# Optimization experiments

Measured on AMD Instinct MI355X. Metric: run time of the kernel, lower is better.

## Reference

```python
import jax, jax.numpy as jnp
import numpy as np

N = 100_000   # nodes
E = 1_600_000 # edges
IN, HID, OUT = 128, 64, 32


def _glorot(key, fan_in, fan_out):
    s = jnp.sqrt(6.0 / (fan_in + fan_out)).astype(jnp.float32)
    return jax.random.uniform(key, (fan_in, fan_out), jnp.float32, -s, s)


def setup_inputs() -> dict:
    key = jax.random.key(0)
    ks = jax.random.split(key, 8)
    x = jax.random.normal(ks[0], (N, IN), jnp.float32)
    edge_index = jax.random.randint(ks[1], (2, E), 0, N, jnp.int64)
    return {
        "x": x,
        "edge_index": edge_index,
        "W1": _glorot(ks[2], IN, HID),
        "b1": jnp.zeros((HID,), jnp.float32),
        "W_mu": _glorot(ks[3], HID, OUT),
        "b_mu": jnp.zeros((OUT,), jnp.float32),
        "W_ls": _glorot(ks[4], HID, OUT),
        "b_ls": jnp.zeros((OUT,), jnp.float32),
    }


def _gcn_conv(x, W, b, src, dst, n, dinv_sqrt):
    """PyG GCNConv: h = x @ W; symmetric-normalized scatter-add incl. self-loops; + b."""
    h = x @ W                                       # [N, F_out]
    coef = dinv_sqrt[src] * dinv_sqrt[dst]          # [E]
    msg = h[src] * coef[:, None]                    # [E, F_out] gather
    agg = jax.ops.segment_sum(msg, dst, num_segments=n)  # scatter-add
    agg = agg + h * (dinv_sqrt * dinv_sqrt)[:, None]      # self-loop contribution
    return agg + b


def reference(x, edge_index, W1, b1, W_mu, b_mu, W_ls, b_ls):
    src, dst = edge_index[0], edge_index[1]
    n = x.shape[0]
    # degree on graph with self-loops (edge weight 1), shared by all three convs
    deg = jax.ops.segment_sum(jnp.ones((src.shape[0],), x.dtype), dst, num_segments=n) + 1.0
    dinv_sqrt = jax.lax.rsqrt(deg)
    h = jax.nn.relu(_gcn_conv(x, W1, b1, src, dst, n, dinv_sqrt))
    mu = _gcn_conv(h, W_mu, b_mu, src, dst, n, dinv_sqrt)
    logstd = _gcn_conv(h, W_ls, b_ls, src, dst, n, dinv_sqrt)
    return mu, logstd
```

## Files before the change

kernel.cpp:

```cpp
#include <hip/hip_runtime.h>
#include <hip/hip_bf16.h>

#define FIN 128
#define HID 64
#define BSN 128
#define BSHIFT 7
#define SRCBITS 20
#define EPB 8192

typedef __attribute__((ext_vector_type(8))) short short8;
typedef __attribute__((ext_vector_type(4))) float floatx4;

__device__ __forceinline__ float bf2f(unsigned short u) {
    union { unsigned int i; float f; } c;
    c.i = ((unsigned int)u) << 16;
    return c.f;
}

__device__ __forceinline__ unsigned short f2bf(float f) {
    union { float f; unsigned int i; } c;
    c.f = f;
    unsigned int u = c.i;
    unsigned int r = (u + 0x7FFFu + ((u >> 16) & 1u)) >> 16;
    return (unsigned short)r;
}

__global__ void bin_count(const int* __restrict__ dst, int* __restrict__ bcnt,
                          int E, int B) {
    __shared__ int hist[1024];
    for (int i = threadIdx.x; i < 1024; i += 256) hist[i] = 0;
    __syncthreads();
    int base = blockIdx.x * EPB;
    int lim = min(base + EPB, E);
    for (int e = base + threadIdx.x; e < lim; e += 256)
        atomicAdd(&hist[dst[e] >> BSHIFT], 1);
    __syncthreads();
    for (int b = threadIdx.x; b < B; b += 256)
        if (hist[b]) atomicAdd(&bcnt[b], hist[b]);
}

__global__ void scan_bkt(int* __restrict__ bcnt, int* __restrict__ bbase,
                         int E, int B) {
    __shared__ int s[1024];
    int t = threadIdx.x;
    int v = (t < B) ? bcnt[t] : 0;
    s[t] = v;
    __syncthreads();
    for (int off = 1; off < 1024; off <<= 1) {
        int a = (t >= off) ? s[t - off] : 0;
        __syncthreads();
        s[t] += a;
        __syncthreads();
    }
    if (t < B) { int ex = s[t] - v; bbase[t] = ex; bcnt[t] = ex; }
    if (t == 0) bbase[B] = E;
}

__global__ void bin_fill(const int* __restrict__ src, const int* __restrict__ dst,
                         int* __restrict__ bcur, unsigned* __restrict__ rec, int E) {
    __shared__ int hist[1024];
    __shared__ int cbase[1024];
    for (int i = threadIdx.x; i < 1024; i += 256) hist[i] = 0;
    __syncthreads();
    int base = blockIdx.x * EPB;
    int lim = min(base + EPB, E);
    for (int e = base + threadIdx.x; e < lim; e += 256)
        atomicAdd(&hist[dst[e] >> BSHIFT], 1);
    __syncthreads();
    for (int b = threadIdx.x; b < 1024; b += 256) {
        int c = hist[b];
        cbase[b] = c ? atomicAdd(&bcur[b], c) : 0;
    }
    __syncthreads();
    for (int i = threadIdx.x; i < 1024; i += 256) hist[i] = 0;
    __syncthreads();
    for (int e = base + threadIdx.x; e < lim; e += 256) {
        int d = dst[e];
        int b = d >> BSHIFT;
        int slot = atomicAdd(&hist[b], 1);
        rec[cbase[b] + slot] = (unsigned)src[e] | ((unsigned)(d & (BSN - 1)) << SRCBITS);
    }
}

__global__ void csr_build(const unsigned* __restrict__ rec, const int* __restrict__ bbase,
                          int* __restrict__ row, int* __restrict__ rend,
                          int* __restrict__ csr, float* __restrict__ dinv, int N) {
    __shared__ int cnt[BSN], excl[BSN], cur[BSN];
    int b = blockIdx.x, t = threadIdx.x;
    if (t < BSN) cnt[t] = 0;
    __syncthreads();
    int start = bbase[b], end = bbase[b + 1];
    for (int i = start + t; i < end; i += 256)
        atomicAdd(&cnt[rec[i] >> SRCBITS], 1);
    __syncthreads();
    if (t < BSN) excl[t] = cnt[t];
    __syncthreads();
    for (int off = 1; off < BSN; off <<= 1) {
        int a = 0;
        if (t < BSN && t >= off) a = excl[t - off];
        __syncthreads();
        if (t < BSN) excl[t] += a;
        __syncthreads();
    }
    if (t < BSN) {
        int inc = excl[t];
        int ex = inc - cnt[t];
        excl[t] = ex;
        cur[t] = 0;
        int n = b * BSN + t;
        if (n < N) {
            row[n]  = start + ex;
            rend[n] = start + inc;
            dinv[n] = rsqrtf((float)cnt[t] + 1.0f);
        }
    }
    __syncthreads();
    for (int i = start + t; i < end; i += 256) {
        unsigned r = rec[i];
        int dl = r >> SRCBITS;
        int slot = atomicAdd(&cur[dl], 1);
        csr[start + excl[dl] + slot] = (int)(r & ((1u << SRCBITS) - 1));
    }
}

__global__ __launch_bounds__(256) void gemm1_mfma(
    const float* __restrict__ x, const float* __restrict__ W1,
    const float* __restrict__ dinv, unsigned short* __restrict__ h0, int N) {
    int wave = threadIdx.x >> 6, lane = threadIdx.x & 63;
    int m = lane & 15, q = lane >> 4;
    short8 bfr[4][4];
#pragma unroll
    for (int ct = 0; ct < 4; ++ct)
#pragma unroll
        for (int kk = 0; kk < 4; ++kk) {
            short8 tf;
#pragma unroll
            for (int jj = 0; jj < 8; ++jj)
                tf[jj] = (short)f2bf(W1[(kk * 32 + q * 8 + jj) * HID + ct * 16 + m]);
            bfr[ct][kk] = tf;
        }
    int ntiles = N >> 4;
    for (int t = blockIdx.x * 4 + wave; t < ntiles; t += gridDim.x * 4) {
        int nbase = t << 4;
        const float* xr = x + (size_t)(nbase + m) * FIN + q * 8;
        short8 afr[4];
#pragma unroll
        for (int kk = 0; kk < 4; ++kk) {
            float4 p0 = *((const float4*)(xr + kk * 32));
            float4 p1 = *((const float4*)(xr + kk * 32 + 4));
            short8 ta;
            ta[0] = (short)f2bf(p0.x); ta[1] = (short)f2bf(p0.y);
            ta[2] = (short)f2bf(p0.z); ta[3] = (short)f2bf(p0.w);
            ta[4] = (short)f2bf(p1.x); ta[5] = (short)f2bf(p1.y);
            ta[6] = (short)f2bf(p1.z); ta[7] = (short)f2bf(p1.w);
            afr[kk] = ta;
        }
        floatx4 cacc[4];
#pragma unroll
        for (int ct = 0; ct < 4; ++ct) cacc[ct] = floatx4{0.f, 0.f, 0.f, 0.f};
#pragma unroll
        for (int ct = 0; ct < 4; ++ct)
#pragma unroll
            for (int kk = 0; kk < 4; ++kk)
                cacc[ct] = __builtin_amdgcn_mfma_f32_16x16x32_bf16(afr[kk], bfr[ct][kk], cacc[ct], 0, 0, 0);
        float4 dv = *((const float4*)(dinv + nbase + q * 4));
#pragma unroll
        for (int ct = 0; ct < 4; ++ct) {
#pragma unroll
            for (int r = 0; r < 4; ++r) {
                float d = (r == 0) ? dv.x : (r == 1) ? dv.y : (r == 2) ? dv.z : dv.w;
                int n = nbase + q * 4 + r;
                h0[(size_t)n * HID + ct * 16 + m] = f2bf(cacc[ct][r] * d);
            }
        }
    }
}

__global__ void pull(const unsigned short* __restrict__ hp,
                     const int* __restrict__ row, const int* __restrict__ rend,
                     const int* __restrict__ csr, const float* __restrict__ dinv,
                     const float* __restrict__ b1,
                     unsigned short* __restrict__ outp, int N, int mode) {
    int wave = threadIdx.x >> 6, lane = threadIdx.x & 63;
    int n = blockIdx.x * 4 + wave;
    if (n >= N) return;
    int start = __builtin_amdgcn_readfirstlane(row[n]);
    int end   = __builtin_amdgcn_readfirstlane(rend[n]);
    float a0 = 0.f, a1 = 0.f, a2 = 0.f, a3 = 0.f;
    float a4 = 0.f, a5 = 0.f, a6 = 0.f, a7 = 0.f;
    int j = start;
    for (; j + 8 <= end; j += 8) {
        int s0 = csr[j],     s1 = csr[j + 1], s2 = csr[j + 2], s3 = csr[j + 3];
        int s4 = csr[j + 4], s5 = csr[j + 5], s6 = csr[j + 6], s7 = csr[j + 7];
        a0 += bf2f(hp[(size_t)s0 * HID + lane]);
        a1 += bf2f(hp[(size_t)s1 * HID + lane]);
        a2 += bf2f(hp[(size_t)s2 * HID + lane]);
        a3 += bf2f(hp[(size_t)s3 * HID + lane]);
        a4 += bf2f(hp[(size_t)s4 * HID + lane]);
        a5 += bf2f(hp[(size_t)s5 * HID + lane]);
        a6 += bf2f(hp[(size_t)s6 * HID + lane]);
        a7 += bf2f(hp[(size_t)s7 * HID + lane]);
    }
    for (; j < end; ++j) {
        int s = csr[j];
        a0 += bf2f(hp[(size_t)s * HID + lane]);
    }
    float acc = ((a0 + a1) + (a2 + a3)) + ((a4 + a5) + (a6 + a7));
    acc += bf2f(hp[(size_t)n * HID + lane]);
    float di = dinv[n];
    float v;
    if (mode == 0) {
        v = di * acc + b1[lane];
        v = v > 0.f ? v : 0.f;
        v *= di;
    } else {
        v = di * acc;
    }
    outp[(size_t)n * HID + lane] = f2bf(v);
}

__global__ __launch_bounds__(256, 4) void gemm2_mfma(
    const unsigned short* __restrict__ abar,
    const float* __restrict__ Wmu, const float* __restrict__ bmu,
    const float* __restrict__ Wls, const float* __restrict__ bls,
    float* __restrict__ out, int N) {
    int wave = threadIdx.x >> 6, lane = threadIdx.x & 63;
    int m = lane & 15, q = lane >> 4;
    short8 bfr[4][2];
#pragma unroll
    for (int ct = 0; ct < 4; ++ct)
#pragma unroll
        for (int kk = 0; kk < 2; ++kk) {
            short8 tf;
#pragma unroll
            for (int jj = 0; jj < 8; ++jj) {
                int k = kk * 32 + q * 8 + jj;
                int col = ct * 16 + m;
                float w = (col < 32) ? Wmu[k * 32 + col] : Wls[k * 32 + (col - 32)];
                tf[jj] = (short)f2bf(w);
            }
            bfr[ct][kk] = tf;
        }
    float bias[4];
#pragma unroll
    for (int ct = 0; ct < 4; ++ct) {
        int col = ct * 16 + m;
        bias[ct] = (col < 32) ? bmu[col] : bls[col - 32];
    }
    int ntiles = N >> 4;
    int gw = blockIdx.x * 4 + wave;
    int nw = gridDim.x * 4;
    for (int t = gw; t < ntiles; t += nw) {
        int nbase = t << 4;
        const unsigned short* arow = abar + (size_t)(nbase + m) * HID;
        short8 a0 = *((const short8*)(arow + q * 8));
        short8 a1 = *((const short8*)(arow + 32 + q * 8));
        floatx4 cacc[4];
#pragma unroll
        for (int ct = 0; ct < 4; ++ct) cacc[ct] = floatx4{0.f, 0.f, 0.f, 0.f};
#pragma unroll
        for (int ct = 0; ct < 4; ++ct) {
            cacc[ct] = __builtin_amdgcn_mfma_f32_16x16x32_bf16(a0, bfr[ct][0], cacc[ct], 0, 0, 0);
            cacc[ct] = __builtin_amdgcn_mfma_f32_16x16x32_bf16(a1, bfr[ct][1], cacc[ct], 0, 0, 0);
        }
#pragma unroll
        for (int ct = 0; ct < 4; ++ct) {
            int col = ct * 16 + m;
            int which = col >> 5, o = col & 31;
#pragma unroll
            for (int r = 0; r < 4; ++r) {
                int n = nbase + q * 4 + r;
                out[(size_t)which * N * 32 + (size_t)n * 32 + o] = cacc[ct][r] + bias[ct];
            }
        }
    }
}

extern "C" void kernel_launch(void* const* d_in, const int* in_sizes, int n_in,
                              void* d_out, int out_size, void* d_ws, size_t ws_size,
                              hipStream_t stream) {
    const float* x   = (const float*)d_in[0];
    const int*   ei  = (const int*)d_in[1];
    const float* W1  = (const float*)d_in[2];
    const float* b1  = (const float*)d_in[3];
    const float* Wmu = (const float*)d_in[4];
    const float* bmu = (const float*)d_in[5];
    const float* Wls = (const float*)d_in[6];
    const float* bls = (const float*)d_in[7];
    int N = in_sizes[0] / FIN;
    int E = in_sizes[1] / 2;
    const int* src = ei;
    const int* dst = ei + E;
    float* out = (float*)d_out;

    int B = (N + BSN - 1) / BSN;
    int nbin = (E + EPB - 1) / EPB;

    float* dinv  = (float*)d_ws;
    int*   row   = (int*)(dinv + N);
    int*   rend  = row + N;
    int*   bbase = rend + N;
    int*   bcur  = bbase + (B + 1);
    int*   csr   = bcur + B;
    unsigned short* bufA = (unsigned short*)(csr + E);
    char* region2 = (char*)(bufA + (size_t)N * HID);
    unsigned* rec        = (unsigned*)region2;
    unsigned short* bufB = (unsigned short*)region2;

    hipMemsetAsync(bcur, 0, (size_t)B * sizeof(int), stream);
    bin_count<<<nbin, 256, 0, stream>>>(dst, bcur, E, B);
    scan_bkt<<<1, 1024, 0, stream>>>(bcur, bbase, E, B);
    bin_fill<<<nbin, 256, 0, stream>>>(src, dst, bcur, rec, E);
    csr_build<<<B, 256, 0, stream>>>(rec, bbase, row, rend, csr, dinv, N);

    gemm1_mfma<<<256, 256, 0, stream>>>(x, W1, dinv, bufA, N);

    int pgrid = (N + 3) / 4;
    pull<<<pgrid, 256, 0, stream>>>(bufA, row, rend, csr, dinv, b1, bufB, N, 0);
    pull<<<pgrid, 256, 0, stream>>>(bufB, row, rend, csr, dinv, b1, bufA, N, 1);

    gemm2_mfma<<<256, 256, 0, stream>>>(bufA, Wmu, bmu, Wls, bls, out, N);
}
```

Before: 307.4 us.

## Vectorize pull gather to 16-byte loads, 8 edges per wave, plus grid tweaks

The pull kernel now splits each wave into 8 row groups of 8 lanes. Each lane loads a 16-byte chunk (8 bf16 features) of a neighbor's row, so one wave gathers 8 edges per load instead of one 2-byte element per lane. Partial sums are reduced across row groups with xor shuffles, and one row group writes the packed output. This cuts the number of memory instructions and index loads in the bandwidth-bound aggregation, at the cost of shuffle reductions and masked tail handling. EPB is halved, and the GEMM grids are doubled to 512 blocks.

```diff
diff --git a/kernel.cpp b/kernel.cpp
--- a/kernel.cpp
+++ b/kernel.cpp
@@ -6,7 +6,7 @@
 #define BSN 128
 #define BSHIFT 7
 #define SRCBITS 20
-#define EPB 8192
+#define EPB 4096
 
 typedef __attribute__((ext_vector_type(8))) short short8;
 typedef __attribute__((ext_vector_type(4))) float floatx4;
@@ -176,47 +176,92 @@
     }
 }
 
-__global__ void pull(const unsigned short* __restrict__ hp,
-                     const int* __restrict__ row, const int* __restrict__ rend,
-                     const int* __restrict__ csr, const float* __restrict__ dinv,
-                     const float* __restrict__ b1,
-                     unsigned short* __restrict__ outp, int N, int mode) {
+
+#define ACC8(a, d)                                                      \
+    do {                                                                \
+        union { unsigned u; float f; } c_;                              \
+        c_.u = (d).x << 16;          a[0] += c_.f;                      \
+        c_.u = (d).x & 0xFFFF0000u;  a[1] += c_.f;                      \
+        c_.u = (d).y << 16;          a[2] += c_.f;                      \
+        c_.u = (d).y & 0xFFFF0000u;  a[3] += c_.f;                      \
+        c_.u = (d).z << 16;          a[4] += c_.f;                      \
+        c_.u = (d).z & 0xFFFF0000u;  a[5] += c_.f;                      \
+        c_.u = (d).w << 16;          a[6] += c_.f;                      \
+        c_.u = (d).w & 0xFFFF0000u;  a[7] += c_.f;                      \
+    } while (0)
+
+__global__ __launch_bounds__(256) void pull(
+    const unsigned short* __restrict__ hp,
+    const int* __restrict__ row, const int* __restrict__ rend,
+    const int* __restrict__ csr, const float* __restrict__ dinv,
+    const float* __restrict__ b1,
+    unsigned short* __restrict__ outp, int N, int mode) {
     int wave = threadIdx.x >> 6, lane = threadIdx.x & 63;
     int n = blockIdx.x * 4 + wave;
     if (n >= N) return;
+    int r = lane >> 3;
+    int g = lane & 7;
     int start = __builtin_amdgcn_readfirstlane(row[n]);
     int end   = __builtin_amdgcn_readfirstlane(rend[n]);
-    float a0 = 0.f, a1 = 0.f, a2 = 0.f, a3 = 0.f;
-    float a4 = 0.f, a5 = 0.f, a6 = 0.f, a7 = 0.f;
+    float4 bb0 = *((const float4*)(b1 + (g << 3)));
+    float4 bb1 = *((const float4*)(b1 + (g << 3) + 4));
+    float a[8] = {0.f, 0.f, 0.f, 0.f, 0.f, 0.f, 0.f, 0.f};
     int j = start;
-    for (; j + 8 <= end; j += 8) {
-        int s0 = csr[j],     s1 = csr[j + 1], s2 = csr[j + 2], s3 = csr[j + 3];
-        int s4 = csr[j + 4], s5 = csr[j + 5], s6 = csr[j + 6], s7 = csr[j + 7];
-        a0 += bf2f(hp[(size_t)s0 * HID + lane]);
-        a1 += bf2f(hp[(size_t)s1 * HID + lane]);
-        a2 += bf2f(hp[(size_t)s2 * HID + lane]);
-        a3 += bf2f(hp[(size_t)s3 * HID + lane]);
-        a4 += bf2f(hp[(size_t)s4 * HID + lane]);
-        a5 += bf2f(hp[(size_t)s5 * HID + lane]);
-        a6 += bf2f(hp[(size_t)s6 * HID + lane]);
-        a7 += bf2f(hp[(size_t)s7 * HID + lane]);
-    }
-    for (; j < end; ++j) {
-        int s = csr[j];
-        a0 += bf2f(hp[(size_t)s * HID + lane]);
-    }
-    float acc = ((a0 + a1) + (a2 + a3)) + ((a4 + a5) + (a6 + a7));
-    acc += bf2f(hp[(size_t)n * HID + lane]);
+    for (; j + 16 <= end; j += 16) {
+        int s0 = csr[j + r];
+        int s1 = csr[j + 8 + r];
+        uint4 d0 = *((const uint4*)(hp + (size_t)s0 * HID + (g << 3)));
+        uint4 d1 = *((const uint4*)(hp + (size_t)s1 * HID + (g << 3)));
+        ACC8(a, d0);
+        ACC8(a, d1);
+    }
+    if (j + 8 <= end) {
+        int s0 = csr[j + r];
+        uint4 d0 = *((const uint4*)(hp + (size_t)s0 * HID + (g << 3)));
+        ACC8(a, d0);
+        j += 8;
+    }
+    if (j < end) {
+        int idx = j + r;
+        int s0 = csr[idx < end ? idx : end - 1];
+        uint4 d0 = *((const uint4*)(hp + (size_t)s0 * HID + (g << 3)));
+        if (idx >= end) { d0.x = 0u; d0.y = 0u; d0.z = 0u; d0.w = 0u; }
+        ACC8(a, d0);
+    }
+#pragma unroll
+    for (int k = 0; k < 8; ++k) {
+        a[k] += __shfl_xor(a[k], 8);
+        a[k] += __shfl_xor(a[k], 16);
+        a[k] += __shfl_xor(a[k], 32);
+    }
+    uint4 sv = *((const uint4*)(hp + (size_t)n * HID + (g << 3)));
+    ACC8(a, sv);
     float di = dinv[n];
-    float v;
+    float v[8];
     if (mode == 0) {
-        v = di * acc + b1[lane];
-        v = v > 0.f ? v : 0.f;
-        v *= di;
+        float bs0 = bb0.x, bs1 = bb0.y, bs2 = bb0.z, bs3 = bb0.w;
+        float bs4 = bb1.x, bs5 = bb1.y, bs6 = bb1.z, bs7 = bb1.w;
+        float t0;
+        t0 = di * a[0] + bs0; v[0] = (t0 > 0.f ? t0 : 0.f) * di;
+        t0 = di * a[1] + bs1; v[1] = (t0 > 0.f ? t0 : 0.f) * di;
+        t0 = di * a[2] + bs2; v[2] = (t0 > 0.f ? t0 : 0.f) * di;
+        t0 = di * a[3] + bs3; v[3] = (t0 > 0.f ? t0 : 0.f) * di;
+        t0 = di * a[4] + bs4; v[4] = (t0 > 0.f ? t0 : 0.f) * di;
+        t0 = di * a[5] + bs5; v[5] = (t0 > 0.f ? t0 : 0.f) * di;
+        t0 = di * a[6] + bs6; v[6] = (t0 > 0.f ? t0 : 0.f) * di;
+        t0 = di * a[7] + bs7; v[7] = (t0 > 0.f ? t0 : 0.f) * di;
     } else {
-        v = di * acc;
-    }
-    outp[(size_t)n * HID + lane] = f2bf(v);
+#pragma unroll
+        for (int k = 0; k < 8; ++k) v[k] = di * a[k];
+    }
+    if (r == 0) {
+        uint4 o;
+        o.x = (unsigned)f2bf(v[0]) | ((unsigned)f2bf(v[1]) << 16);
+        o.y = (unsigned)f2bf(v[2]) | ((unsigned)f2bf(v[3]) << 16);
+        o.z = (unsigned)f2bf(v[4]) | ((unsigned)f2bf(v[5]) << 16);
+        o.w = (unsigned)f2bf(v[6]) | ((unsigned)f2bf(v[7]) << 16);
+        *((uint4*)(outp + (size_t)n * HID + (g << 3))) = o;
+    }
 }
 
 __global__ __launch_bounds__(256, 4) void gemm2_mfma(
@@ -313,11 +358,11 @@
     bin_fill<<<nbin, 256, 0, stream>>>(src, dst, bcur, rec, E);
     csr_build<<<B, 256, 0, stream>>>(rec, bbase, row, rend, csr, dinv, N);
 
-    gemm1_mfma<<<256, 256, 0, stream>>>(x, W1, dinv, bufA, N);
+    gemm1_mfma<<<512, 256, 0, stream>>>(x, W1, dinv, bufA, N);
 
     int pgrid = (N + 3) / 4;
     pull<<<pgrid, 256, 0, stream>>>(bufA, row, rend, csr, dinv, b1, bufB, N, 0);
     pull<<<pgrid, 256, 0, stream>>>(bufB, row, rend, csr, dinv, b1, bufA, N, 1);
 
-    gemm2_mfma<<<256, 256, 0, stream>>>(bufA, Wmu, bmu, Wls, bls, out, N);
-}
+    gemm2_mfma<<<512, 256, 0, stream>>>(bufA, Wmu, bmu, Wls, bls, out, N);
+}
```

Result: faster. 291.4 us (-5.2%).
